# Performance work log

Measured on AMD Instinct MI355X. Metric: run time of the kernel, lower is better.

Reference implementation:

```python
import jax, jax.numpy as jnp
import numpy as np

NUM_HEADS = 8
CHUNK = 64


def _retention(q, k, v):
    # q, k: (B, H, L, DK); v: (B, H, L, DV). Chunked linear retention with
    # per-head exponential decay gamma_h = 1 - 2^(-5-h) (RetNet convention).
    B, Hn, L, DK = q.shape
    DV = v.shape[-1]
    C = CHUNK
    N = L // C
    dt = q.dtype
    gamma = (1.0 - jnp.exp2(-5.0 - jnp.arange(Hn, dtype=jnp.float32))).astype(dt)  # (H,)
    q = q * (DK ** -0.5)
    idx = jnp.arange(C)
    diff = idx[:, None] - idx[None, :]
    # intra-chunk causal decay mask D[h,i,j] = gamma_h^(i-j) for i>=j else 0
    D = jnp.where(diff >= 0, gamma[:, None, None] ** diff, 0.0).astype(dt)      # (H,C,C)
    decay_q = (gamma[:, None] ** (idx[None, :] + 1)).astype(dt)                 # (H,C)
    decay_k = (gamma[:, None] ** (C - 1 - idx[None, :])).astype(dt)             # (H,C)
    decay_s = (gamma ** C).astype(dt)                                           # (H,)

    def to_chunks(x):
        return jnp.moveaxis(x.reshape(B, Hn, N, C, -1), 2, 0)  # (N,B,H,C,d)

    qs, ks, vs = map(to_chunks, (q, k, v))

    def step(S, x):
        qc, kc, vc = x  # (B,H,C,dk) / (B,H,C,dv)
        attn = jnp.einsum('bhid,bhjd->bhij', qc, kc) * D
        o_intra = jnp.einsum('bhij,bhje->bhie', attn, vc)
        o_inter = jnp.einsum('bhid,bhde->bhie', qc * decay_q[None, :, :, None], S)
        S_new = decay_s[None, :, None, None] * S + jnp.einsum(
            'bhjd,bhje->bhde', kc * decay_k[None, :, :, None], vc)
        return S_new, o_intra + o_inter

    S0 = jnp.zeros((B, Hn, DK, DV), dt)
    _, o = jax.lax.scan(step, S0, (qs, ks, vs))  # (N,B,H,C,DV)
    return jnp.moveaxis(o, 0, 2).reshape(B, Hn, L, DV)


def _xavier(key, fan_in, fan_out, gain=2 ** (-2.5)):
    limit = gain * np.sqrt(6.0 / (fan_in + fan_out))
    return jax.random.uniform(key, (fan_in, fan_out), jnp.float32, -limit, limit)


def setup_inputs() -> dict:
    key = jax.random.key(0)
    k0, k1, k2, k3, k4 = jax.random.split(key, 5)
    B, L, D = 2, 4096, 1024
    return {
        'hidden_states': jax.random.normal(k0, (B, L, D), jnp.float32),
        'rel_pos': jnp.zeros((1,), jnp.float32),  # unused by the module's forward
        'Wq': _xavier(k1, D, D),
        'Wk': _xavier(k2, D, D),
        'Wv': _xavier(k3, D, D),
        'Wo': _xavier(k4, D, D),
    }


def reference(hidden_states, rel_pos, Wq, Wk, Wv, Wo):
    B, L, Dm = hidden_states.shape
    Hd = Dm // NUM_HEADS
    q = (hidden_states @ Wq).reshape(B, L, NUM_HEADS, Hd).transpose(0, 2, 1, 3)
    k = (hidden_states @ Wk).reshape(B, L, NUM_HEADS, Hd).transpose(0, 2, 1, 3)
    v = (hidden_states @ Wv).reshape(B, L, NUM_HEADS, Hd).transpose(0, 2, 1, 3)
    o = _retention(q, k, v)  # (B,H,L,Hd)
    o = o.transpose(0, 2, 1, 3).reshape(B, L, Dm)
    return o @ Wo
```

## Files before the change

### kernel.cpp

```cpp
#include <hip/hip_runtime.h>
#include <hip/hip_bf16.h>

typedef __bf16 bf16;
typedef __bf16 bf16x8 __attribute__((ext_vector_type(8)));
typedef float f32x4 __attribute__((ext_vector_type(4)));

#define MFMA16(a, b, c) __builtin_amdgcn_mfma_f32_16x16x32_bf16((a), (b), (c), 0, 0, 0)


__device__ __forceinline__ void g2l16(const bf16* g, bf16* l) {
  __builtin_amdgcn_global_load_lds(
      (const __attribute__((address_space(1))) void*)g,
      (__attribute__((address_space(3))) void*)l, 16, 0, 0);
}

__global__ __launch_bounds__(256) void prep(
    const float* __restrict__ X, const float* __restrict__ Wq,
    const float* __restrict__ Wk, const float* __restrict__ Wv,
    const float* __restrict__ Wo, bf16* __restrict__ Wt,
    bf16* __restrict__ Xb) {
  const int tid = threadIdx.x;
  if (blockIdx.z == 4) {
#pragma unroll
    for (int it = 0; it < 16; ++it) {
      const size_t i = (((size_t)blockIdx.x * 16 + it) * 256 + tid) * 8;
      float4 a = *(const float4*)&X[i];
      float4 b = *(const float4*)&X[i + 4];
      union { bf16 h[8]; uint4 u; } p;
      p.h[0] = (bf16)a.x; p.h[1] = (bf16)a.y; p.h[2] = (bf16)a.z; p.h[3] = (bf16)a.w;
      p.h[4] = (bf16)b.x; p.h[5] = (bf16)b.y; p.h[6] = (bf16)b.z; p.h[7] = (bf16)b.w;
      *(uint4*)&Xb[i] = p.u;
    }
    return;
  }
  __shared__ bf16 t[64 * 72];
  const float* src = (blockIdx.z == 0) ? Wq : (blockIdx.z == 1) ? Wk
                     : (blockIdx.z == 2) ? Wv : Wo;
  bf16* dst = Wt + (size_t)blockIdx.z * 1024 * 1024;
  const int k0 = (blockIdx.x >> 4) * 64, n0 = (blockIdx.x & 15) * 64;
#pragma unroll
  for (int s = 0; s < 4; ++s) {
    int u = tid + s * 256;
    int r = u >> 4, c4 = (u & 15) * 4;
    float4 f = *(const float4*)&src[(size_t)(k0 + r) * 1024 + n0 + c4];
    t[r * 72 + c4 + 0] = (bf16)f.x;
    t[r * 72 + c4 + 1] = (bf16)f.y;
    t[r * 72 + c4 + 2] = (bf16)f.z;
    t[r * 72 + c4 + 3] = (bf16)f.w;
  }
  __syncthreads();
#pragma unroll
  for (int s = 0; s < 2; ++s) {
    int u = tid + s * 256;
    int r = u >> 3, cc = u & 7;
    union { bf16 h[8]; uint4 u4; } pk;
#pragma unroll
    for (int j = 0; j < 8; ++j) pk.h[j] = t[(cc * 8 + j) * 72 + r];
    *(uint4*)&dst[(size_t)(n0 + r) * 1024 + k0 + cc * 8] = pk.u4;
  }
}

template <typename TC, int MODE>
__global__ __launch_bounds__(256) void gemm_lds(
    const bf16* __restrict__ A, const bf16* __restrict__ Bt,
    TC* __restrict__ C, bf16* __restrict__ kTb, bf16* __restrict__ vTb,
    float alpha) {
  __shared__ bf16 lA[128 * 64];
  __shared__ bf16 lB[128 * 64];
  const int m0 = blockIdx.x * 128, n0 = blockIdx.y * 128;
  if (MODE) {
    Bt += (size_t)blockIdx.z * 1024 * 1024;
    if (blockIdx.z != 0) alpha = 1.0f;
  }
  const int tid = threadIdx.x;
  const int w = tid >> 6, lane = tid & 63, lr = lane & 15, quad = lane >> 4;
  const int wm = w >> 1, wn = w & 1;

  const int srow = w * 32 + (lane >> 3);
  const int clog = (lane & 7) ^ ((lane >> 3) & 7);
  const bf16* gA = A + (size_t)(m0 + srow) * 1024 + clog * 8;
  const bf16* gB = Bt + (size_t)(n0 + srow) * 1024 + clog * 8;

  f32x4 acc[4][4] = {};

  for (int it = 0; it < 16; ++it) {
    const int k0 = it * 64;
#pragma unroll
    for (int is = 0; is < 4; ++is) {
      g2l16(gA + (size_t)is * 8 * 1024 + k0, &lA[(w * 32 + is * 8) * 64]);
      g2l16(gB + (size_t)is * 8 * 1024 + k0, &lB[(w * 32 + is * 8) * 64]);
    }
    __syncthreads();
#pragma unroll
    for (int kk = 0; kk < 2; ++kk) {
      bf16x8 af[4], bfv[4];
#pragma unroll
      for (int i = 0; i < 4; ++i) {
        const int m = wm * 64 + i * 16 + lr;
        af[i] = *(bf16x8*)&lA[m * 64 + (((kk * 4 + quad) ^ (lr & 7)) * 8)];
      }
#pragma unroll
      for (int j = 0; j < 4; ++j) {
        const int n = wn * 64 + j * 16 + lr;
        bfv[j] = *(bf16x8*)&lB[n * 64 + (((kk * 4 + quad) ^ (lr & 7)) * 8)];
      }
#pragma unroll
      for (int i = 0; i < 4; ++i)
#pragma unroll
        for (int j = 0; j < 4; ++j)
          acc[i][j] = MFMA16(af[i], bfv[j], acc[i][j]);
    }
    __syncthreads();
  }
#pragma unroll
  for (int i = 0; i < 4; ++i) {
#pragma unroll
    for (int j = 0; j < 4; ++j) {
      const int row = m0 + wm * 64 + i * 16 + quad * 4;
      const int col = n0 + wn * 64 + j * 16 + lr;
      if (MODE == 0 || blockIdx.z < 2) {
        TC* Cz = C + (MODE ? (size_t)blockIdx.z * 8192 * 1024 : 0);
#pragma unroll
        for (int r = 0; r < 4; ++r)
          Cz[(size_t)(row + r) * 1024 + col] = (TC)(acc[i][j][r] * alpha);
      }
      if (MODE == 1 && blockIdx.z >= 1) {
        bf16* Tp = (blockIdx.z == 1) ? kTb : vTb;
        const int b = row >> 12, pos = row & 4095;
        const int n = pos >> 6, c0 = pos & 63;
        const int h = col >> 7, d = col & 127;
        union { bf16 h4[4]; uint2 u2; } pk;
#pragma unroll
        for (int r = 0; r < 4; ++r) pk.h4[r] = (bf16)acc[i][j][r];
        *(uint2*)&Tp[((size_t)((b * 8 + h) * 64 + n)) * 8192 + d * 64 + c0] = pk.u2;
      }
    }
  }
}

__global__ __launch_bounds__(256) void chunk_kv(
    const bf16* __restrict__ kT, const bf16* __restrict__ vT,
    bf16* __restrict__ Tb) {
  __shared__ bf16 lK[128 * 64];
  __shared__ bf16 lV[128 * 64];
  const int g = blockIdx.x;
  const int h = (g >> 6) & 7;
  const float lg = log2f(1.0f - exp2f(-5.0f - (float)h));
  const float ginv = exp2f(-lg);
  const int tid = threadIdx.x;
  const bf16* ks = kT + (size_t)g * 8192;
  const bf16* vs = vT + (size_t)g * 8192;
#pragma unroll
  for (int s = 0; s < 4; ++s) {
    int u = tid + s * 256;
    int d = u >> 3, c0 = (u & 7) * 8;
    int pc = ((u & 7) ^ (d & 7)) * 8;
    *(uint4*)&lV[d * 64 + pc] = *(const uint4*)&vs[d * 64 + c0];
    union { uint4 u4; bf16 h8[8]; } kv;
    kv.u4 = *(const uint4*)&ks[d * 64 + c0];
    float e = exp2f((float)(63 - c0) * lg);
    union { bf16 h8[8]; uint4 u4; } o;
#pragma unroll
    for (int jj = 0; jj < 8; ++jj) {
      o.h8[jj] = (bf16)((float)kv.h8[jj] * e);
      e *= ginv;
    }
    *(uint4*)&lK[d * 64 + pc] = o.u4;
  }
  __syncthreads();
  const int w = tid >> 6, lane = tid & 63, lr = lane & 15, quad = lane >> 4;
  const int wm = w >> 1, wn = w & 1;
  f32x4 acc[4][4] = {};
#pragma unroll
  for (int kk = 0; kk < 2; ++kk) {
    const int pc = ((kk * 4 + quad) ^ (lr & 7)) * 8;
    bf16x8 af[4], bv[4];
#pragma unroll
    for (int i = 0; i < 4; ++i)
      af[i] = *(bf16x8*)&lK[(wm * 64 + i * 16 + lr) * 64 + pc];
#pragma unroll
    for (int j = 0; j < 4; ++j)
      bv[j] = *(bf16x8*)&lV[(wn * 64 + j * 16 + lr) * 64 + pc];
#pragma unroll
    for (int i = 0; i < 4; ++i)
#pragma unroll
      for (int j = 0; j < 4; ++j)
        acc[i][j] = MFMA16(af[i], bv[j], acc[i][j]);
  }
  bf16* tchunk = Tb + (size_t)g * 16384;
#pragma unroll
  for (int i = 0; i < 4; ++i) {
#pragma unroll
    for (int j = 0; j < 4; ++j) {
      const int dk = wm * 64 + i * 16 + quad * 4;
      const int dv = wn * 64 + j * 16 + lr;
      union { bf16 h4[4]; uint2 u2; } pk;
#pragma unroll
      for (int r = 0; r < 4; ++r) pk.h4[r] = (bf16)acc[i][j][r];
      *(uint2*)&tchunk[(size_t)dv * 128 + dk] = pk.u2;
    }
  }
}

__global__ __launch_bounds__(256) void scan_state(bf16* __restrict__ Tb) {
  const int blk = blockIdx.x;
  const int bh = blk >> 4, h = bh & 7;
  const float gs = exp2f(64.0f * log2f(1.0f - exp2f(-5.0f - (float)h)));
  const size_t base =
      (size_t)bh * 1048576 + (size_t)(blk & 15) * 1024 + threadIdx.x * 4;
  float S0 = 0.0f, S1 = 0.0f, S2 = 0.0f, S3 = 0.0f;
#pragma unroll 8
  for (int n = 0; n < 64; ++n) {
    const size_t a = base + (size_t)n * 16384;
    union { uint2 u; bf16 h4[4]; } t, o;
    t.u = *(const uint2*)&Tb[a];
    o.h4[0] = (bf16)S0; o.h4[1] = (bf16)S1;
    o.h4[2] = (bf16)S2; o.h4[3] = (bf16)S3;
    *(uint2*)&Tb[a] = o.u;
    S0 = gs * S0 + (float)t.h4[0];
    S1 = gs * S1 + (float)t.h4[1];
    S2 = gs * S2 + (float)t.h4[2];
    S3 = gs * S3 + (float)t.h4[3];
  }
}

__global__ __launch_bounds__(256) void chunk_out(
    const bf16* __restrict__ qb, const bf16* __restrict__ kb,
    const bf16* __restrict__ vT, const bf16* __restrict__ Sp,
    bf16* __restrict__ ob) {
  __shared__ bf16 lQ[64 * 136];
  __shared__ bf16 lVt[128 * 64];
  __shared__ bf16 lP[64 * 72];
  const int g = blockIdx.x;
  const int bh = g >> 6, n = g & 63, b = bh >> 3, h = bh & 7;
  const float lg = log2f(1.0f - exp2f(-5.0f - (float)h));
  const float gam = exp2f(lg);
  const int tid = threadIdx.x;
  const size_t rowbase = (size_t)(b * 4096 + n * 64) * 1024 + h * 128;
  const bf16* qc = qb + rowbase;
  const bf16* kc = kb + rowbase;
  const bf16* vs = vT + (size_t)g * 8192;
#pragma unroll
  for (int s = 0; s < 4; ++s) {
    int u = tid + s * 256;
    int c = u >> 4, d0 = (u & 15) * 8;
    *(uint4*)&lQ[c * 136 + d0] = *(const uint4*)&qc[(size_t)c * 1024 + d0];
    int d = u >> 3, cc = (u & 7) * 8;
    int pc = ((u & 7) ^ (d & 7)) * 8;
    *(uint4*)&lVt[d * 64 + pc] = *(const uint4*)&vs[d * 64 + cc];
  }
  __syncthreads();
  const int w = tid >> 6, lane = tid & 63, lr = lane & 15, quad = lane >> 4;

  f32x4 p[4] = {};
#pragma unroll
  for (int kk = 0; kk < 4; ++kk) {
    bf16x8 bfrag =
        *(const bf16x8*)&kc[(size_t)(w * 16 + lr) * 1024 + kk * 32 + quad * 8];
#pragma unroll
    for (int i = 0; i < 4; ++i) {
      bf16x8 afrag = *(bf16x8*)&lQ[(i * 16 + lr) * 136 + kk * 32 + quad * 8];
      p[i] = MFMA16(afrag, bfrag, p[i]);
    }
  }
#pragma unroll
  for (int i = 0; i < 4; ++i) {
#pragma unroll
    for (int r = 0; r < 4; ++r) {
      const int row = i * 16 + quad * 4 + r;
      const int col = w * 16 + lr;
      const int diff = row - col;
      const float val = (diff >= 0) ? p[i][r] * exp2f((float)diff * lg) : 0.0f;
      lP[row * 72 + col] = (bf16)val;
    }
  }
  __syncthreads();

  f32x4 oac[4][2] = {}, oin[4][2] = {};
#pragma unroll
  for (int j = 0; j < 2; ++j) {
#pragma unroll
    for (int kk = 0; kk < 2; ++kk) {
      const int m = w * 32 + j * 16 + lr;
      bf16x8 bfrag = *(bf16x8*)&lVt[m * 64 + (((kk * 4 + quad) ^ (m & 7)) * 8)];
#pragma unroll
      for (int i = 0; i < 4; ++i) {
        bf16x8 afrag = *(bf16x8*)&lP[(i * 16 + lr) * 72 + kk * 32 + quad * 8];
        oac[i][j] = MFMA16(afrag, bfrag, oac[i][j]);
      }
    }
  }
  const bf16* sp = Sp + (size_t)g * 16384;
#pragma unroll
  for (int kk = 0; kk < 4; ++kk) {
    bf16x8 af[4];
#pragma unroll
    for (int i = 0; i < 4; ++i)
      af[i] = *(bf16x8*)&lQ[(i * 16 + lr) * 136 + kk * 32 + quad * 8];
#pragma unroll
    for (int j = 0; j < 2; ++j) {
      bf16x8 bfrag =
          *(const bf16x8*)&sp[(size_t)(w * 32 + j * 16 + lr) * 128 + kk * 32 + quad * 8];
#pragma unroll
      for (int i = 0; i < 4; ++i) oin[i][j] = MFMA16(af[i], bfrag, oin[i][j]);
    }
  }

  bf16* oc = ob + rowbase;
#pragma unroll
  for (int i = 0; i < 4; ++i) {
    const float d0 = exp2f((float)(i * 16 + quad * 4 + 1) * lg);
#pragma unroll
    for (int j = 0; j < 2; ++j) {
      float d = d0;
#pragma unroll
      for (int r = 0; r < 4; ++r) {
        const int row = i * 16 + quad * 4 + r;
        const int col = w * 32 + j * 16 + lr;
        oc[(size_t)row * 1024 + col] = (bf16)(oac[i][j][r] + d * oin[i][j][r]);
        d *= gam;
      }
    }
  }
}

extern "C" void kernel_launch(void* const* d_in, const int* in_sizes, int n_in,
                              void* d_out, int out_size, void* d_ws,
                              size_t ws_size, hipStream_t stream) {
  const float* X  = (const float*)d_in[0];
  const float* Wq = (const float*)d_in[2];
  const float* Wk = (const float*)d_in[3];
  const float* Wv = (const float*)d_in[4];
  const float* Wo = (const float*)d_in[5];

  char* ws = (char*)d_ws;
  const size_t MB = 1024 * 1024;
  bf16* qb  = (bf16*)(ws);
  bf16* kb  = (bf16*)(ws + 16 * MB);
  bf16* kTb = (bf16*)(ws + 32 * MB);
  bf16* vTb = (bf16*)(ws + 48 * MB);
  bf16* Tb  = (bf16*)(ws + 64 * MB);
  bf16* Wt  = (bf16*)(ws + 96 * MB);
  bf16* Xb  = (bf16*)(ws + 104 * MB);
  bf16* ob  = Xb;

  prep<<<dim3(256, 1, 5), 256, 0, stream>>>(X, Wq, Wk, Wv, Wo, Wt, Xb);

  const float qscale = 0.08838834764831845f;
  gemm_lds<bf16, 1><<<dim3(64, 8, 3), 256, 0, stream>>>(Xb, Wt, qb, kTb, vTb,
                                                        qscale);

  chunk_kv<<<1024, 256, 0, stream>>>(kTb, vTb, Tb);
  scan_state<<<256, 256, 0, stream>>>(Tb);
  chunk_out<<<1024, 256, 0, stream>>>(qb, kb, vTb, Tb, ob);

  gemm_lds<float, 0><<<dim3(64, 8), 256, 0, stream>>>(
      ob, Wt + (size_t)3 * 1024 * 1024, (float*)d_out, nullptr, nullptr, 1.0f);
}
```

Baseline: 232.6 us.

## Stage transposed K/V epilogue through LDS and drop row-major K buffer

```diff
diff --git a/kernel.cpp b/kernel.cpp
--- a/kernel.cpp
+++ b/kernel.cpp
@@ -65,13 +65,11 @@
     const bf16* __restrict__ A, const bf16* __restrict__ Bt,
     TC* __restrict__ C, bf16* __restrict__ kTb, bf16* __restrict__ vTb,
     float alpha) {
-  __shared__ bf16 lA[128 * 64];
-  __shared__ bf16 lB[128 * 64];
+  __shared__ bf16 smem[16384];
+  bf16* lA = smem;
+  bf16* lB = smem + 8192;
   const int m0 = blockIdx.x * 128, n0 = blockIdx.y * 128;
-  if (MODE) {
-    Bt += (size_t)blockIdx.z * 1024 * 1024;
-    if (blockIdx.z != 0) alpha = 1.0f;
-  }
+  if (MODE) Bt += (size_t)blockIdx.z * 1024 * 1024;
   const int tid = threadIdx.x;
   const int w = tid >> 6, lane = tid & 63, lr = lane & 15, quad = lane >> 4;
   const int wm = w >> 1, wn = w & 1;
@@ -112,28 +110,45 @@
     }
     __syncthreads();
   }
-#pragma unroll
-  for (int i = 0; i < 4; ++i) {
-#pragma unroll
-    for (int j = 0; j < 4; ++j) {
-      const int row = m0 + wm * 64 + i * 16 + quad * 4;
-      const int col = n0 + wn * 64 + j * 16 + lr;
-      if (MODE == 0 || blockIdx.z < 2) {
-        TC* Cz = C + (MODE ? (size_t)blockIdx.z * 8192 * 1024 : 0);
+
+  if (MODE == 0 || blockIdx.z == 0) {
+#pragma unroll
+    for (int i = 0; i < 4; ++i) {
+#pragma unroll
+      for (int j = 0; j < 4; ++j) {
+        const int row = m0 + wm * 64 + i * 16 + quad * 4;
+        const int col = n0 + wn * 64 + j * 16 + lr;
 #pragma unroll
         for (int r = 0; r < 4; ++r)
-          Cz[(size_t)(row + r) * 1024 + col] = (TC)(acc[i][j][r] * alpha);
-      }
-      if (MODE == 1 && blockIdx.z >= 1) {
-        bf16* Tp = (blockIdx.z == 1) ? kTb : vTb;
-        const int b = row >> 12, pos = row & 4095;
-        const int n = pos >> 6, c0 = pos & 63;
-        const int h = col >> 7, d = col & 127;
+          C[(size_t)(row + r) * 1024 + col] = (TC)(acc[i][j][r] * alpha);
+      }
+    }
+  } else {
+    bf16* Tp = (blockIdx.z == 1) ? kTb : vTb;
+#pragma unroll
+    for (int i = 0; i < 4; ++i) {
+#pragma unroll
+      for (int j = 0; j < 4; ++j) {
+        const int d = wn * 64 + j * 16 + lr;
+        const int c0 = i * 16 + quad * 4;
+        const int ph = ((c0 >> 3) ^ (d & 7)) * 8 + (c0 & 7);
         union { bf16 h4[4]; uint2 u2; } pk;
 #pragma unroll
         for (int r = 0; r < 4; ++r) pk.h4[r] = (bf16)acc[i][j][r];
-        *(uint2*)&Tp[((size_t)((b * 8 + h) * 64 + n)) * 8192 + d * 64 + c0] = pk.u2;
-      }
+        *(uint2*)&smem[wm * 8192 + d * 64 + ph] = pk.u2;
+      }
+    }
+    __syncthreads();
+    const int h = n0 >> 7;
+#pragma unroll
+    for (int s = 0; s < 8; ++s) {
+      const int p = tid + s * 256;
+      const int c8 = p & 7, d = (p >> 3) & 127, ch = p >> 10;
+      uint4 vdat = *(uint4*)&smem[ch * 8192 + d * 64 + ((c8 ^ (d & 7)) * 8)];
+      const int row0 = m0 + ch * 64;
+      const int b = row0 >> 12, n = (row0 & 4095) >> 6;
+      *(uint4*)&Tp[((size_t)((b * 8 + h) * 64 + n)) * 8192 + d * 64 + c8 * 8] =
+          vdat;
     }
   }
 }
@@ -225,12 +240,12 @@
 }
 
 __global__ __launch_bounds__(256) void chunk_out(
-    const bf16* __restrict__ qb, const bf16* __restrict__ kb,
+    const bf16* __restrict__ qb, const bf16* __restrict__ kT,
     const bf16* __restrict__ vT, const bf16* __restrict__ Sp,
     bf16* __restrict__ ob) {
-  __shared__ bf16 lQ[64 * 136];
-  __shared__ bf16 lVt[128 * 64];
-  __shared__ bf16 lP[64 * 72];
+  __shared__ bf16 lK[128 * 64];
+  __shared__ bf16 lV[128 * 64];
+  __shared__ bf16 lP[64 * 64];
   const int g = blockIdx.x;
   const int bh = g >> 6, n = g & 63, b = bh >> 3, h = bh & 7;
   const float lg = log2f(1.0f - exp2f(-5.0f - (float)h));
@@ -238,29 +253,36 @@
   const int tid = threadIdx.x;
   const size_t rowbase = (size_t)(b * 4096 + n * 64) * 1024 + h * 128;
   const bf16* qc = qb + rowbase;
-  const bf16* kc = kb + rowbase;
+  const bf16* ks = kT + (size_t)g * 8192;
   const bf16* vs = vT + (size_t)g * 8192;
 #pragma unroll
   for (int s = 0; s < 4; ++s) {
     int u = tid + s * 256;
-    int c = u >> 4, d0 = (u & 15) * 8;
-    *(uint4*)&lQ[c * 136 + d0] = *(const uint4*)&qc[(size_t)c * 1024 + d0];
-    int d = u >> 3, cc = (u & 7) * 8;
-    int pc = ((u & 7) ^ (d & 7)) * 8;
-    *(uint4*)&lVt[d * 64 + pc] = *(const uint4*)&vs[d * 64 + cc];
+    int d = u >> 3, c8 = u & 7;
+    *(uint4*)&lK[d * 64 + ((c8 ^ ((d + (d >> 3)) & 7)) * 8)] =
+        *(const uint4*)&ks[d * 64 + c8 * 8];
+    *(uint4*)&lV[d * 64 + ((c8 ^ (d & 7)) * 8)] =
+        *(const uint4*)&vs[d * 64 + c8 * 8];
   }
   __syncthreads();
   const int w = tid >> 6, lane = tid & 63, lr = lane & 15, quad = lane >> 4;
 
   f32x4 p[4] = {};
+  const int cj = w * 16 + lr;
 #pragma unroll
   for (int kk = 0; kk < 4; ++kk) {
-    bf16x8 bfrag =
-        *(const bf16x8*)&kc[(size_t)(w * 16 + lr) * 1024 + kk * 32 + quad * 8];
+    union { bf16 h8[8]; bf16x8 v; } bf;
+#pragma unroll
+    for (int e = 0; e < 8; ++e) {
+      const int d = kk * 32 + quad * 8 + e;
+      bf.h8[e] =
+          lK[d * 64 + (((cj >> 3) ^ ((d + (d >> 3)) & 7)) * 8) + (cj & 7)];
+    }
 #pragma unroll
     for (int i = 0; i < 4; ++i) {
-      bf16x8 afrag = *(bf16x8*)&lQ[(i * 16 + lr) * 136 + kk * 32 + quad * 8];
-      p[i] = MFMA16(afrag, bfrag, p[i]);
+      bf16x8 afrag =
+          *(const bf16x8*)&qc[(size_t)(i * 16 + lr) * 1024 + kk * 32 + quad * 8];
+      p[i] = MFMA16(afrag, bf.v, p[i]);
     }
   }
 #pragma unroll
@@ -268,10 +290,9 @@
 #pragma unroll
     for (int r = 0; r < 4; ++r) {
       const int row = i * 16 + quad * 4 + r;
-      const int col = w * 16 + lr;
-      const int diff = row - col;
+      const int diff = row - cj;
       const float val = (diff >= 0) ? p[i][r] * exp2f((float)diff * lg) : 0.0f;
-      lP[row * 72 + col] = (bf16)val;
+      lP[row * 64 + (((cj >> 3) ^ (row & 7)) * 8) + (cj & 7)] = (bf16)val;
     }
   }
   __syncthreads();
@@ -282,10 +303,12 @@
 #pragma unroll
     for (int kk = 0; kk < 2; ++kk) {
       const int m = w * 32 + j * 16 + lr;
-      bf16x8 bfrag = *(bf16x8*)&lVt[m * 64 + (((kk * 4 + quad) ^ (m & 7)) * 8)];
+      bf16x8 bfrag = *(bf16x8*)&lV[m * 64 + (((kk * 4 + quad) ^ (m & 7)) * 8)];
 #pragma unroll
       for (int i = 0; i < 4; ++i) {
-        bf16x8 afrag = *(bf16x8*)&lP[(i * 16 + lr) * 72 + kk * 32 + quad * 8];
+        const int row = i * 16 + lr;
+        bf16x8 afrag =
+            *(bf16x8*)&lP[row * 64 + (((kk * 4 + quad) ^ (row & 7)) * 8)];
         oac[i][j] = MFMA16(afrag, bfrag, oac[i][j]);
       }
     }
@@ -296,11 +319,12 @@
     bf16x8 af[4];
 #pragma unroll
     for (int i = 0; i < 4; ++i)
-      af[i] = *(bf16x8*)&lQ[(i * 16 + lr) * 136 + kk * 32 + quad * 8];
+      af[i] =
+          *(const bf16x8*)&qc[(size_t)(i * 16 + lr) * 1024 + kk * 32 + quad * 8];
 #pragma unroll
     for (int j = 0; j < 2; ++j) {
-      bf16x8 bfrag =
-          *(const bf16x8*)&sp[(size_t)(w * 32 + j * 16 + lr) * 128 + kk * 32 + quad * 8];
+      bf16x8 bfrag = *(const bf16x8*)&sp[(size_t)(w * 32 + j * 16 + lr) * 128 +
+                                         kk * 32 + quad * 8];
 #pragma unroll
       for (int i = 0; i < 4; ++i) oin[i][j] = MFMA16(af[i], bfrag, oin[i][j]);
     }
@@ -336,12 +360,11 @@
   char* ws = (char*)d_ws;
   const size_t MB = 1024 * 1024;
   bf16* qb  = (bf16*)(ws);
-  bf16* kb  = (bf16*)(ws + 16 * MB);
-  bf16* kTb = (bf16*)(ws + 32 * MB);
-  bf16* vTb = (bf16*)(ws + 48 * MB);
-  bf16* Tb  = (bf16*)(ws + 64 * MB);
-  bf16* Wt  = (bf16*)(ws + 96 * MB);
-  bf16* Xb  = (bf16*)(ws + 104 * MB);
+  bf16* kTb = (bf16*)(ws + 16 * MB);
+  bf16* vTb = (bf16*)(ws + 32 * MB);
+  bf16* Tb  = (bf16*)(ws + 48 * MB);
+  bf16* Wt  = (bf16*)(ws + 80 * MB);
+  bf16* Xb  = (bf16*)(ws + 88 * MB);
   bf16* ob  = Xb;
 
   prep<<<dim3(256, 1, 5), 256, 0, stream>>>(X, Wq, Wk, Wv, Wo, Wt, Xb);
@@ -352,7 +375,7 @@
 
   chunk_kv<<<1024, 256, 0, stream>>>(kTb, vTb, Tb);
   scan_state<<<256, 256, 0, stream>>>(Tb);
-  chunk_out<<<1024, 256, 0, stream>>>(qb, kb, vTb, Tb, ob);
+  chunk_out<<<1024, 256, 0, stream>>>(qb, kTb, vTb, Tb, ob);
 
   gemm_lds<float, 0><<<dim3(64, 8), 256, 0, stream>>>(
       ob, Wt + (size_t)3 * 1024 * 1024, (float*)d_out, nullptr, nullptr, 1.0f);
```

Result: slower. 242.8 us (+4.4%).

## Fuse chunk state, scan, and output into one recurrent retention kernel

Applied to the files above, without the earlier changes.

```diff
diff --git a/kernel.cpp b/kernel.cpp
--- a/kernel.cpp
+++ b/kernel.cpp
@@ -138,189 +138,175 @@
   }
 }
 
-__global__ __launch_bounds__(256) void chunk_kv(
-    const bf16* __restrict__ kT, const bf16* __restrict__ vT,
-    bf16* __restrict__ Tb) {
-  __shared__ bf16 lK[128 * 64];
-  __shared__ bf16 lV[128 * 64];
-  const int g = blockIdx.x;
-  const int h = (g >> 6) & 7;
+__global__ __launch_bounds__(256) void retention(
+    const bf16* __restrict__ qb, const bf16* __restrict__ kb,
+    const bf16* __restrict__ kTb, const bf16* __restrict__ vTb,
+    bf16* __restrict__ ob) {
+  __shared__ bf16 sKT[2][128 * 64];
+  __shared__ bf16 sVT[2][64 * 64];
+  __shared__ bf16 sS[64 * 128];
+  __shared__ bf16 sP[64 * 64];
+  const int blk = blockIdx.x, bh = blk >> 1, dvh = blk & 1;
+  const int b = bh >> 3, h = bh & 7;
   const float lg = log2f(1.0f - exp2f(-5.0f - (float)h));
-  const float ginv = exp2f(-lg);
+  const float g64 = exp2f(64.0f * lg), gam = exp2f(lg), ginv = exp2f(-lg);
   const int tid = threadIdx.x;
-  const bf16* ks = kT + (size_t)g * 8192;
-  const bf16* vs = vT + (size_t)g * 8192;
-#pragma unroll
-  for (int s = 0; s < 4; ++s) {
-    int u = tid + s * 256;
-    int d = u >> 3, c0 = (u & 7) * 8;
-    int pc = ((u & 7) ^ (d & 7)) * 8;
-    *(uint4*)&lV[d * 64 + pc] = *(const uint4*)&vs[d * 64 + c0];
-    union { uint4 u4; bf16 h8[8]; } kv;
-    kv.u4 = *(const uint4*)&ks[d * 64 + c0];
-    float e = exp2f((float)(63 - c0) * lg);
-    union { bf16 h8[8]; uint4 u4; } o;
-#pragma unroll
-    for (int jj = 0; jj < 8; ++jj) {
-      o.h8[jj] = (bf16)((float)kv.h8[jj] * e);
-      e *= ginv;
-    }
-    *(uint4*)&lK[d * 64 + pc] = o.u4;
+  const int w = tid >> 6, lane = tid & 63, lr = lane & 15, quad = lane >> 4;
+
+  for (int i = tid; i < 1024; i += 256) ((uint4*)sS)[i] = make_uint4(0, 0, 0, 0);
+
+  f32x4 ST[8] = {};
+  uint4 pk[4], pv[2];
+
+  {
+    const bf16* kg = kTb + (size_t)(bh * 64 + 0) * 8192;
+    const bf16* vg = vTb + (size_t)(bh * 64 + 0) * 8192 + dvh * 4096;
+#pragma unroll
+    for (int s = 0; s < 4; ++s) {
+      int idx = tid + s * 256;
+      pk[s] = *(const uint4*)&kg[(idx >> 3) * 64 + (idx & 7) * 8];
+    }
+#pragma unroll
+    for (int s = 0; s < 2; ++s) {
+      int idx = tid + s * 256;
+      pv[s] = *(const uint4*)&vg[(idx >> 3) * 64 + (idx & 7) * 8];
+    }
+#pragma unroll
+    for (int s = 0; s < 4; ++s) {
+      int idx = tid + s * 256, d = idx >> 3, c8 = idx & 7;
+      union { uint4 u4; bf16 h8[8]; } kv; kv.u4 = pk[s];
+      float e = exp2f((float)(63 - c8 * 8) * lg);
+      union { bf16 h8[8]; uint4 u4; } o;
+#pragma unroll
+      for (int jj = 0; jj < 8; ++jj) { o.h8[jj] = (bf16)((float)kv.h8[jj] * e); e *= ginv; }
+      *(uint4*)&sKT[0][d * 64 + ((c8 ^ (d & 7)) * 8)] = o.u4;
+    }
+#pragma unroll
+    for (int s = 0; s < 2; ++s) {
+      int idx = tid + s * 256, d = idx >> 3, c8 = idx & 7;
+      *(uint4*)&sVT[0][d * 64 + ((c8 ^ (d & 7)) * 8)] = pv[s];
+    }
   }
   __syncthreads();
-  const int w = tid >> 6, lane = tid & 63, lr = lane & 15, quad = lane >> 4;
-  const int wm = w >> 1, wn = w & 1;
-  f32x4 acc[4][4] = {};
-#pragma unroll
-  for (int kk = 0; kk < 2; ++kk) {
-    const int pc = ((kk * 4 + quad) ^ (lr & 7)) * 8;
-    bf16x8 af[4], bv[4];
-#pragma unroll
-    for (int i = 0; i < 4; ++i)
-      af[i] = *(bf16x8*)&lK[(wm * 64 + i * 16 + lr) * 64 + pc];
-#pragma unroll
-    for (int j = 0; j < 4; ++j)
-      bv[j] = *(bf16x8*)&lV[(wn * 64 + j * 16 + lr) * 64 + pc];
-#pragma unroll
-    for (int i = 0; i < 4; ++i)
-#pragma unroll
-      for (int j = 0; j < 4; ++j)
-        acc[i][j] = MFMA16(af[i], bv[j], acc[i][j]);
-  }
-  bf16* tchunk = Tb + (size_t)g * 16384;
-#pragma unroll
-  for (int i = 0; i < 4; ++i) {
-#pragma unroll
-    for (int j = 0; j < 4; ++j) {
-      const int dk = wm * 64 + i * 16 + quad * 4;
-      const int dv = wn * 64 + j * 16 + lr;
-      union { bf16 h4[4]; uint2 u2; } pk;
-#pragma unroll
-      for (int r = 0; r < 4; ++r) pk.h4[r] = (bf16)acc[i][j][r];
-      *(uint2*)&tchunk[(size_t)dv * 128 + dk] = pk.u2;
-    }
-  }
-}
-
-__global__ __launch_bounds__(256) void scan_state(bf16* __restrict__ Tb) {
-  const int blk = blockIdx.x;
-  const int bh = blk >> 4, h = bh & 7;
-  const float gs = exp2f(64.0f * log2f(1.0f - exp2f(-5.0f - (float)h)));
-  const size_t base =
-      (size_t)bh * 1048576 + (size_t)(blk & 15) * 1024 + threadIdx.x * 4;
-  float S0 = 0.0f, S1 = 0.0f, S2 = 0.0f, S3 = 0.0f;
-#pragma unroll 8
+
   for (int n = 0; n < 64; ++n) {
-    const size_t a = base + (size_t)n * 16384;
-    union { uint2 u; bf16 h4[4]; } t, o;
-    t.u = *(const uint2*)&Tb[a];
-    o.h4[0] = (bf16)S0; o.h4[1] = (bf16)S1;
-    o.h4[2] = (bf16)S2; o.h4[3] = (bf16)S3;
-    *(uint2*)&Tb[a] = o.u;
-    S0 = gs * S0 + (float)t.h4[0];
-    S1 = gs * S1 + (float)t.h4[1];
-    S2 = gs * S2 + (float)t.h4[2];
-    S3 = gs * S3 + (float)t.h4[3];
-  }
-}
-
-__global__ __launch_bounds__(256) void chunk_out(
-    const bf16* __restrict__ qb, const bf16* __restrict__ kb,
-    const bf16* __restrict__ vT, const bf16* __restrict__ Sp,
-    bf16* __restrict__ ob) {
-  __shared__ bf16 lQ[64 * 136];
-  __shared__ bf16 lVt[128 * 64];
-  __shared__ bf16 lP[64 * 72];
-  const int g = blockIdx.x;
-  const int bh = g >> 6, n = g & 63, b = bh >> 3, h = bh & 7;
-  const float lg = log2f(1.0f - exp2f(-5.0f - (float)h));
-  const float gam = exp2f(lg);
-  const int tid = threadIdx.x;
-  const size_t rowbase = (size_t)(b * 4096 + n * 64) * 1024 + h * 128;
-  const bf16* qc = qb + rowbase;
-  const bf16* kc = kb + rowbase;
-  const bf16* vs = vT + (size_t)g * 8192;
-#pragma unroll
-  for (int s = 0; s < 4; ++s) {
-    int u = tid + s * 256;
-    int c = u >> 4, d0 = (u & 15) * 8;
-    *(uint4*)&lQ[c * 136 + d0] = *(const uint4*)&qc[(size_t)c * 1024 + d0];
-    int d = u >> 3, cc = (u & 7) * 8;
-    int pc = ((u & 7) ^ (d & 7)) * 8;
-    *(uint4*)&lVt[d * 64 + pc] = *(const uint4*)&vs[d * 64 + cc];
-  }
-  __syncthreads();
-  const int w = tid >> 6, lane = tid & 63, lr = lane & 15, quad = lane >> 4;
-
-  f32x4 p[4] = {};
-#pragma unroll
-  for (int kk = 0; kk < 4; ++kk) {
-    bf16x8 bfrag =
-        *(const bf16x8*)&kc[(size_t)(w * 16 + lr) * 1024 + kk * 32 + quad * 8];
+    const int buf = n & 1;
+    {
+      const int np = (n < 63) ? n + 1 : 63;
+      const bf16* kg = kTb + (size_t)(bh * 64 + np) * 8192;
+      const bf16* vg = vTb + (size_t)(bh * 64 + np) * 8192 + dvh * 4096;
+#pragma unroll
+      for (int s = 0; s < 4; ++s) {
+        int idx = tid + s * 256;
+        pk[s] = *(const uint4*)&kg[(idx >> 3) * 64 + (idx & 7) * 8];
+      }
+#pragma unroll
+      for (int s = 0; s < 2; ++s) {
+        int idx = tid + s * 256;
+        pv[s] = *(const uint4*)&vg[(idx >> 3) * 64 + (idx & 7) * 8];
+      }
+    }
+    const size_t rowbase = (size_t)(b * 4096 + n * 64) * 1024 + h * 128;
+    const bf16* qc = qb + rowbase;
+    const bf16* kc = kb + rowbase;
+
+    f32x4 oin[4] = {}, oac[4] = {};
+#pragma unroll
+    for (int kk = 0; kk < 4; ++kk) {
+      bf16x8 bS = *(bf16x8*)&sS[(w * 16 + lr) * 128 + (((kk * 4 + quad) ^ (lr & 7)) * 8)];
+#pragma unroll
+      for (int i = 0; i < 4; ++i) {
+        bf16x8 aq = *(const bf16x8*)&qc[(size_t)(i * 16 + lr) * 1024 + kk * 32 + quad * 8];
+        oin[i] = MFMA16(aq, bS, oin[i]);
+      }
+    }
+
+    f32x4 p[4] = {};
+#pragma unroll
+    for (int kk = 0; kk < 4; ++kk) {
+      bf16x8 bk = *(const bf16x8*)&kc[(size_t)(w * 16 + lr) * 1024 + kk * 32 + quad * 8];
+#pragma unroll
+      for (int i = 0; i < 4; ++i) {
+        bf16x8 aq = *(const bf16x8*)&qc[(size_t)(i * 16 + lr) * 1024 + kk * 32 + quad * 8];
+        p[i] = MFMA16(aq, bk, p[i]);
+      }
+    }
+    const int cj = w * 16 + lr;
 #pragma unroll
     for (int i = 0; i < 4; ++i) {
-      bf16x8 afrag = *(bf16x8*)&lQ[(i * 16 + lr) * 136 + kk * 32 + quad * 8];
-      p[i] = MFMA16(afrag, bfrag, p[i]);
-    }
-  }
-#pragma unroll
-  for (int i = 0; i < 4; ++i) {
-#pragma unroll
-    for (int r = 0; r < 4; ++r) {
-      const int row = i * 16 + quad * 4 + r;
-      const int col = w * 16 + lr;
-      const int diff = row - col;
-      const float val = (diff >= 0) ? p[i][r] * exp2f((float)diff * lg) : 0.0f;
-      lP[row * 72 + col] = (bf16)val;
-    }
-  }
-  __syncthreads();
-
-  f32x4 oac[4][2] = {}, oin[4][2] = {};
-#pragma unroll
-  for (int j = 0; j < 2; ++j) {
-#pragma unroll
-    for (int kk = 0; kk < 2; ++kk) {
-      const int m = w * 32 + j * 16 + lr;
-      bf16x8 bfrag = *(bf16x8*)&lVt[m * 64 + (((kk * 4 + quad) ^ (m & 7)) * 8)];
-#pragma unroll
-      for (int i = 0; i < 4; ++i) {
-        bf16x8 afrag = *(bf16x8*)&lP[(i * 16 + lr) * 72 + kk * 32 + quad * 8];
-        oac[i][j] = MFMA16(afrag, bfrag, oac[i][j]);
-      }
-    }
-  }
-  const bf16* sp = Sp + (size_t)g * 16384;
-#pragma unroll
-  for (int kk = 0; kk < 4; ++kk) {
-    bf16x8 af[4];
-#pragma unroll
-    for (int i = 0; i < 4; ++i)
-      af[i] = *(bf16x8*)&lQ[(i * 16 + lr) * 136 + kk * 32 + quad * 8];
-#pragma unroll
-    for (int j = 0; j < 2; ++j) {
-      bf16x8 bfrag =
-          *(const bf16x8*)&sp[(size_t)(w * 32 + j * 16 + lr) * 128 + kk * 32 + quad * 8];
-#pragma unroll
-      for (int i = 0; i < 4; ++i) oin[i][j] = MFMA16(af[i], bfrag, oin[i][j]);
-    }
-  }
-
-  bf16* oc = ob + rowbase;
-#pragma unroll
-  for (int i = 0; i < 4; ++i) {
-    const float d0 = exp2f((float)(i * 16 + quad * 4 + 1) * lg);
-#pragma unroll
-    for (int j = 0; j < 2; ++j) {
-      float d = d0;
 #pragma unroll
       for (int r = 0; r < 4; ++r) {
         const int row = i * 16 + quad * 4 + r;
-        const int col = w * 32 + j * 16 + lr;
-        oc[(size_t)row * 1024 + col] = (bf16)(oac[i][j][r] + d * oin[i][j][r]);
+        const int diff = row - cj;
+        const float val = (diff >= 0) ? p[i][r] * exp2f((float)diff * lg) : 0.0f;
+        sP[row * 64 + (((cj >> 3) ^ (row & 7)) * 8) + (cj & 7)] = (bf16)val;
+      }
+    }
+    __syncthreads();
+
+#pragma unroll
+    for (int kk = 0; kk < 2; ++kk) {
+      bf16x8 bV = *(bf16x8*)&sVT[buf][(w * 16 + lr) * 64 + (((kk * 4 + quad) ^ (lr & 7)) * 8)];
+#pragma unroll
+      for (int i = 0; i < 4; ++i) {
+        bf16x8 aP = *(bf16x8*)&sP[(i * 16 + lr) * 64 + (((kk * 4 + quad) ^ (lr & 7)) * 8)];
+        oac[i] = MFMA16(aP, bV, oac[i]);
+      }
+    }
+
+#pragma unroll
+    for (int nt = 0; nt < 8; ++nt) {
+#pragma unroll
+      for (int r = 0; r < 4; ++r) ST[nt][r] *= g64;
+    }
+#pragma unroll
+    for (int kk2 = 0; kk2 < 2; ++kk2) {
+      bf16x8 aV = *(bf16x8*)&sVT[buf][(w * 16 + lr) * 64 + (((kk2 * 4 + quad) ^ (lr & 7)) * 8)];
+#pragma unroll
+      for (int nt = 0; nt < 8; ++nt) {
+        bf16x8 bK = *(bf16x8*)&sKT[buf][(nt * 16 + lr) * 64 + (((kk2 * 4 + quad) ^ (lr & 7)) * 8)];
+        ST[nt] = MFMA16(aV, bK, ST[nt]);
+      }
+    }
+#pragma unroll
+    for (int nt = 0; nt < 8; ++nt) {
+#pragma unroll
+      for (int r = 0; r < 4; ++r) {
+        const int dv = w * 16 + quad * 4 + r;
+        const int dk = nt * 16 + lr;
+        sS[dv * 128 + (((dk >> 3) ^ (dv & 7)) * 8) + (dk & 7)] = (bf16)ST[nt][r];
+      }
+    }
+
+    bf16* oc = ob + rowbase + dvh * 64 + w * 16;
+#pragma unroll
+    for (int i = 0; i < 4; ++i) {
+      float d = exp2f((float)(i * 16 + quad * 4 + 1) * lg);
+#pragma unroll
+      for (int r = 0; r < 4; ++r) {
+        const int row = i * 16 + quad * 4 + r;
+        oc[(size_t)row * 1024 + lr] = (bf16)(oac[i][r] + d * oin[i][r]);
         d *= gam;
       }
     }
+
+    const int nb = buf ^ 1;
+#pragma unroll
+    for (int s = 0; s < 4; ++s) {
+      int idx = tid + s * 256, d = idx >> 3, c8 = idx & 7;
+      union { uint4 u4; bf16 h8[8]; } kv; kv.u4 = pk[s];
+      float e = exp2f((float)(63 - c8 * 8) * lg);
+      union { bf16 h8[8]; uint4 u4; } o;
+#pragma unroll
+      for (int jj = 0; jj < 8; ++jj) { o.h8[jj] = (bf16)((float)kv.h8[jj] * e); e *= ginv; }
+      *(uint4*)&sKT[nb][d * 64 + ((c8 ^ (d & 7)) * 8)] = o.u4;
+    }
+#pragma unroll
+    for (int s = 0; s < 2; ++s) {
+      int idx = tid + s * 256, d = idx >> 3, c8 = idx & 7;
+      *(uint4*)&sVT[nb][d * 64 + ((c8 ^ (d & 7)) * 8)] = pv[s];
+    }
+    __syncthreads();
   }
 }
 
@@ -339,9 +325,8 @@
   bf16* kb  = (bf16*)(ws + 16 * MB);
   bf16* kTb = (bf16*)(ws + 32 * MB);
   bf16* vTb = (bf16*)(ws + 48 * MB);
-  bf16* Tb  = (bf16*)(ws + 64 * MB);
-  bf16* Wt  = (bf16*)(ws + 96 * MB);
-  bf16* Xb  = (bf16*)(ws + 104 * MB);
+  bf16* Wt  = (bf16*)(ws + 64 * MB);
+  bf16* Xb  = (bf16*)(ws + 72 * MB);
   bf16* ob  = Xb;
 
   prep<<<dim3(256, 1, 5), 256, 0, stream>>>(X, Wq, Wk, Wv, Wo, Wt, Xb);
@@ -350,9 +335,7 @@
   gemm_lds<bf16, 1><<<dim3(64, 8, 3), 256, 0, stream>>>(Xb, Wt, qb, kTb, vTb,
                                                         qscale);
 
-  chunk_kv<<<1024, 256, 0, stream>>>(kTb, vTb, Tb);
-  scan_state<<<256, 256, 0, stream>>>(Tb);
-  chunk_out<<<1024, 256, 0, stream>>>(qb, kb, vTb, Tb, ob);
+  retention<<<32, 256, 0, stream>>>(qb, kb, kTb, vTb, ob);
 
   gemm_lds<float, 0><<<dim3(64, 8), 256, 0, stream>>>(
       ob, Wt + (size_t)3 * 1024 * 1024, (float*)d_out, nullptr, nullptr, 1.0f);
```

Measured after the change: 459.1 us. +97.4%, slower.
